# Kernel tuning notes

Measured on AMD Instinct MI355X. Metric: run time of the kernel, lower is better.

Reference implementation:

```python
import jax, jax.numpy as jnp
import numpy as np

C = 256
NUM_HEADS = 8
GROUPS = 8
EPS = 1e-5


def setup_inputs() -> dict:
    key = jax.random.key(0)
    ks = jax.random.split(key, 7)
    B, H, W = 2, 64, 64
    x = jax.random.normal(ks[0], (B, C, H, W), dtype=jnp.float32)
    gn_weight = jnp.ones((C,), dtype=jnp.float32)
    gn_bias = jnp.zeros((C,), dtype=jnp.float32)
    # 1x1 convs == per-pixel linear layers
    w_qkv = jax.random.normal(ks[1], (3 * C, C), dtype=jnp.float32) * (1.0 / np.sqrt(C))
    b_qkv = jax.random.normal(ks[2], (3 * C,), dtype=jnp.float32) * 0.01
    w_proj = jax.random.normal(ks[3], (C, C), dtype=jnp.float32) * (1.0 / np.sqrt(C))
    b_proj = jax.random.normal(ks[4], (C,), dtype=jnp.float32) * 0.01
    return {"x": x, "gn_weight": gn_weight, "gn_bias": gn_bias,
            "w_qkv": w_qkv, "b_qkv": b_qkv, "w_proj": w_proj, "b_proj": b_proj}


def reference(x, gn_weight, gn_bias, w_qkv, b_qkv, w_proj, b_proj):
    B, Cc, H, W = x.shape
    nh = NUM_HEADS
    hd = Cc // nh
    N = H * W
    scale = hd ** (-0.5)

    # GroupNorm(8, C): normalize over (C/G, H, W) per group, biased variance
    xg = x.reshape(B, GROUPS, Cc // GROUPS, H, W)
    mean = xg.mean(axis=(2, 3, 4), keepdims=True)
    var = xg.var(axis=(2, 3, 4), keepdims=True)
    hn = (xg - mean) * jax.lax.rsqrt(var + EPS)
    hn = hn.reshape(B, Cc, H, W) * gn_weight[None, :, None, None] + gn_bias[None, :, None, None]

    hf = hn.reshape(B, Cc, N)                       # [B, C, N]
    qkv = jnp.einsum('oc,bcn->bon', w_qkv, hf) + b_qkv[None, :, None]  # [B, 3C, N]
    qkv = qkv.reshape(B, 3, nh, hd, N)
    # q,k,v: [B, nh, N, hd]
    q = jnp.transpose(qkv[:, 0], (0, 1, 3, 2))
    k = jnp.transpose(qkv[:, 1], (0, 1, 3, 2))
    v = jnp.transpose(qkv[:, 2], (0, 1, 3, 2))

    attn = jnp.einsum('bhqd,bhkd->bhqk', q, k) * scale  # [B, nh, N, N]
    attn = jax.nn.softmax(attn, axis=-1)
    o = jnp.einsum('bhqk,bhkd->bhqd', attn, v)           # [B, nh, N, hd]
    o = jnp.transpose(o, (0, 1, 3, 2)).reshape(B, Cc, H, W)

    of = o.reshape(B, Cc, N)
    out = jnp.einsum('oc,bcn->bon', w_proj, of) + b_proj[None, :, None]
    return out.reshape(B, Cc, H, W)
```

## Files before the change

### kernel.cpp

```cpp
#include <hip/hip_runtime.h>


typedef _Float16 half8 __attribute__((ext_vector_type(8)));
typedef __fp16   fp16x2 __attribute__((ext_vector_type(2)));
typedef float    f32x4 __attribute__((ext_vector_type(4)));
typedef int      int2v __attribute__((ext_vector_type(2)));
typedef int      int4v __attribute__((ext_vector_type(4)));

__device__ __forceinline__ f32x4 mfma16(half8 a, half8 b, f32x4 c) {
  return __builtin_amdgcn_mfma_f32_16x16x32_f16(a, b, c, 0, 0, 0);
}

#if __has_builtin(__builtin_amdgcn_exp2f)
#define EXP2(x) __builtin_amdgcn_exp2f(x)
#else
#define EXP2(x) exp2f(x)
#endif

__device__ __forceinline__ unsigned short h_bits(_Float16 h) {
  return __builtin_bit_cast(unsigned short, h);
}
__device__ __forceinline__ int h2_bits(fp16x2 h) {
  return __builtin_bit_cast(int, h);
}

constexpr float CSCALE = (float)(1.4426950408889634 / 5.656854249492381);

__global__ __launch_bounds__(256) void gn_stats(const float* __restrict__ x,
                                                float* __restrict__ stats) {
  const int bg = blockIdx.x, ch = blockIdx.y, tid = threadIdx.x;
  const float* p = x + (size_t)bg * 131072 + (size_t)ch * 4096;
  float s = 0.f, ss = 0.f;
#pragma unroll
  for (int j = 0; j < 4; ++j) {
    f32x4 v = *(const f32x4*)(p + j * 1024 + tid * 4);
#pragma unroll
    for (int k = 0; k < 4; ++k) { s += v[k]; ss += v[k] * v[k]; }
  }
#pragma unroll
  for (int m = 1; m <= 32; m <<= 1) { s += __shfl_xor(s, m); ss += __shfl_xor(ss, m); }
  __shared__ float red[8];
  const int wv = tid >> 6;
  if ((tid & 63) == 0) { red[wv * 2] = s; red[wv * 2 + 1] = ss; }
  __syncthreads();
  if (tid == 0) {
    float S = red[0] + red[2] + red[4] + red[6];
    float SS = red[1] + red[3] + red[5] + red[7];
    atomicAdd(&stats[bg * 2], S);
    atomicAdd(&stats[bg * 2 + 1], SS);
  }
}

__global__ __launch_bounds__(256) void gn_apply(const float* __restrict__ x,
                                                const float* __restrict__ gw,
                                                const float* __restrict__ gb,
                                                const float* __restrict__ stats,
                                                _Float16* __restrict__ hn) {
  __shared__ float tile[64 * 65];
  const int tid = threadIdx.x;
  const int a = tid & 15;
  const int row16 = tid >> 4;
  const int b = blockIdx.z, c0 = blockIdx.y * 64, n0 = blockIdx.x * 64;
#pragma unroll
  for (int m = 0; m < 4; ++m) {
    const int cl = row16 + 16 * m;
    const int c = c0 + cl;
    const int g = c >> 5;
    const float s = stats[(b * 8 + g) * 2];
    const float ss = stats[(b * 8 + g) * 2 + 1];
    const float mean = s * (1.f / 131072.f);
    const float var = ss * (1.f / 131072.f) - mean * mean;
    const float rstd = rsqrtf(var + 1e-5f);
    const float ga = gw[c] * rstd;
    const float be = gb[c] - mean * ga;
    f32x4 xv = *(const f32x4*)(x + ((size_t)(b * 256 + c)) * 4096 + n0 + a * 4);
#pragma unroll
    for (int j = 0; j < 4; ++j) tile[cl * 65 + a * 4 + j] = xv[j] * ga + be;
  }
  __syncthreads();
#pragma unroll
  for (int m = 0; m < 4; ++m) {
    const int nl = row16 + 16 * m;
    const int cb = a * 4;
    int2v uh;
    unsigned short hh[4];
#pragma unroll
    for (int j = 0; j < 4; ++j) {
      hh[j] = h_bits((_Float16)tile[(cb + j) * 65 + nl]);
    }
    uh[0] = hh[0] | (hh[1] << 16); uh[1] = hh[2] | (hh[3] << 16);
    size_t off = ((size_t)(b * 4096 + n0 + nl)) * 256 + c0 + cb;
    *(int2v*)(hn + off) = uh;
  }
}

__global__ __launch_bounds__(256) void wcast(const float* __restrict__ wq,
                                             const float* __restrict__ wp,
                                             _Float16* __restrict__ wqh,
                                             _Float16* __restrict__ wph) {
  const int idx = blockIdx.x * 256 + threadIdx.x;
  if (idx < 196608) {
    wqh[idx] = (_Float16)wq[idx];
  } else {
    wph[idx - 196608] = (_Float16)wp[idx - 196608];
  }
}

template <int MODE>
__global__ __launch_bounds__(256) void gemm_f16(
    const _Float16* __restrict__ W, const _Float16* __restrict__ Bm,
    const float* __restrict__ bias,
    _Float16* __restrict__ qkT, _Float16* __restrict__ v_t,
    float* __restrict__ outp) {
  __shared__ _Float16 a_lds[2][4096];
  __shared__ _Float16 b_lds[2][4096];
  const int tid = threadIdx.x, lane = tid & 63, wv = tid >> 6;
  const int qq = lane >> 4, ii = lane & 15;
  const int m0 = blockIdx.x * 64, n0 = blockIdx.y * 64, bz = blockIdx.z;

  const _Float16* asrc[2];
  const _Float16* bsrc[2];
  int dst8[2];
#pragma unroll
  for (int rep = 0; rep < 2; ++rep) {
    const int idx = tid + 256 * rep;
    dst8[rep] = idx * 8;
    const int j = idx >> 7, c = (idx >> 6) & 1, l = idx & 63;
    const int lq = l >> 4, li = l & 15;
    asrc[rep] = W + (size_t)(m0 + 16 * j + li) * 256 + 32 * c + 8 * lq;
    bsrc[rep] = Bm + ((size_t)(bz * 4096 + n0 + 16 * j + li)) * 256 + 32 * c + 8 * lq;
  }

  f32x4 acc[4] = {};

  half8 ar0 = *(const half8*)asrc[0];
  half8 ar1 = *(const half8*)asrc[1];
  half8 br0 = *(const half8*)bsrc[0];
  half8 br1 = *(const half8*)bsrc[1];
  *(half8*)(a_lds[0] + dst8[0]) = ar0;
  *(half8*)(a_lds[0] + dst8[1]) = ar1;
  *(half8*)(b_lds[0] + dst8[0]) = br0;
  *(half8*)(b_lds[0] + dst8[1]) = br1;
  __syncthreads();

  for (int it = 0; it < 4; ++it) {
    const int cur = it & 1;
    if (it < 3) {
      const int ko = (it + 1) * 64;
      ar0 = *(const half8*)(asrc[0] + ko);
      ar1 = *(const half8*)(asrc[1] + ko);
      br0 = *(const half8*)(bsrc[0] + ko);
      br1 = *(const half8*)(bsrc[1] + ko);
    }
    half8 ah0 = *(const half8*)(a_lds[cur] + ((wv * 2 + 0) * 64 + lane) * 8);
    half8 ah1 = *(const half8*)(a_lds[cur] + ((wv * 2 + 1) * 64 + lane) * 8);
#pragma unroll
    for (int t = 0; t < 4; ++t) {
      half8 b0 = *(const half8*)(b_lds[cur] + ((t * 2 + 0) * 64 + lane) * 8);
      half8 b1 = *(const half8*)(b_lds[cur] + ((t * 2 + 1) * 64 + lane) * 8);
      acc[t] = mfma16(ah0, b0, acc[t]);
      acc[t] = mfma16(ah1, b1, acc[t]);
    }
    if (it < 3) {
      _Float16* an = a_lds[cur ^ 1];
      _Float16* bn = b_lds[cur ^ 1];
      *(half8*)(an + dst8[0]) = ar0;
      *(half8*)(an + dst8[1]) = ar1;
      *(half8*)(bn + dst8[0]) = br0;
      *(half8*)(bn + dst8[1]) = br1;
    }
    __syncthreads();
  }

  const int och0 = m0 + 16 * wv + 4 * qq;
  if (MODE == 0) {
    if (m0 < 512) {
      const float sc = (m0 < 256) ? CSCALE : 1.0f;
#pragma unroll
      for (int t = 0; t < 4; ++t) {
        const int n = n0 + 16 * t + ii;
        unsigned short hh[4];
#pragma unroll
        for (int r = 0; r < 4; ++r) {
          hh[r] = h_bits((_Float16)((acc[t][r] + bias[och0 + r]) * sc));
        }
        int2v u;
        u[0] = hh[0] | (hh[1] << 16);
        u[1] = hh[2] | (hh[3] << 16);
        *(int2v*)(qkT + ((size_t)(bz * 4096 + n)) * 512 + och0) = u;
      }
    } else {
#pragma unroll
      for (int t = 0; t < 4; ++t) {
#pragma unroll
        for (int r = 0; r < 4; ++r) {
          const int och = och0 + r;
          const int d = och - 512;
          const int hd_ = d & 31, head = d >> 5;
          const int n = n0 + 16 * t + ii;
          v_t[((size_t)((bz * 8 + head) * 32 + hd_)) * 4096 + n] =
              (_Float16)(acc[t][r] + bias[och]);
        }
      }
    }
  } else {
#pragma unroll
    for (int t = 0; t < 4; ++t) {
#pragma unroll
      for (int r = 0; r < 4; ++r) {
        const int och = och0 + r;
        const int n = n0 + 16 * t + ii;
        outp[((size_t)(bz * 256 + och)) * 4096 + n] = acc[t][r] + bias[och];
      }
    }
  }
}

__global__ __launch_bounds__(256) void attn_kernel(
    const _Float16* __restrict__ qkT, const _Float16* __restrict__ v_t,
    float* __restrict__ opart, float* __restrict__ lpart) {
  __shared__ _Float16 k_lds[2][4096];
  __shared__ _Float16 v_lds[2][4096];
  const int tid = threadIdx.x, lane = tid & 63, wv = tid >> 6;
  const int qq = lane >> 4, ii = lane & 15;
  const int bh = blockIdx.y, b = bh >> 3, h = bh & 7;
  const int n0 = blockIdx.x * 128;
  const int part = blockIdx.z;
  const int key0 = part * 2048;

  const _Float16* qbase =
      qkT + ((size_t)(b * 4096 + n0 + 32 * wv + ii)) * 512 + h * 32 + 8 * qq;
  half8 qf0 = *(const half8*)qbase;
  half8 qf1 = *(const half8*)(qbase + (size_t)16 * 512);

  const _Float16* ksrc[2];
  const _Float16* vsrc[2];
  int dst8[2];
#pragma unroll
  for (int rep = 0; rep < 2; ++rep) {
    const int idx = tid + 256 * rep;
    dst8[rep] = idx * 8;
    const int f = idx >> 6, l = idx & 63;
    const int fq = l >> 4, fi = l & 15;
    const int u = f >> 1, hf = f & 1;
    const int g = 32 * u + 4 * hf + 8 * (fi >> 2) + (fi & 3);
    ksrc[rep] = qkT + ((size_t)(b * 4096 + key0 + g)) * 512 + 256 + h * 32 + 8 * fq;
    vsrc[rep] = v_t + ((size_t)(bh * 32 + 16 * hf + fi)) * 4096 + key0 + 32 * u + 8 * fq;
  }

  half8 ones8;
#pragma unroll
  for (int j = 0; j < 8; ++j) ones8[j] = (_Float16)1.0f;

  f32x4 o00 = {}, o10 = {}, o01 = {}, o11 = {}, accl0 = {}, accl1 = {};

  half8 kr0 = *(const half8*)ksrc[0];
  half8 kr1 = *(const half8*)ksrc[1];
  half8 vr0 = *(const half8*)vsrc[0];
  half8 vr1 = *(const half8*)vsrc[1];
  *(half8*)(k_lds[0] + dst8[0]) = kr0;
  *(half8*)(k_lds[0] + dst8[1]) = kr1;
  *(half8*)(v_lds[0] + dst8[0]) = vr0;
  *(half8*)(v_lds[0] + dst8[1]) = vr1;
  __syncthreads();

  for (int kb = 0; kb < 16; ++kb) {
    const int cur = kb & 1;
    if (kb < 15) {
      const size_t ko = (size_t)(kb + 1) * 128 * 512;
      const size_t vo = (size_t)(kb + 1) * 128;
      kr0 = *(const half8*)(ksrc[0] + ko);
      kr1 = *(const half8*)(ksrc[1] + ko);
      vr0 = *(const half8*)(vsrc[0] + vo);
      vr1 = *(const half8*)(vsrc[1] + vo);
    }
    const _Float16* kbase = k_lds[cur];
    const _Float16* vbase = v_lds[cur];

#pragma unroll
    for (int u = 0; u < 4; ++u) {
      half8 kfa = *(const half8*)(kbase + u * 1024 + lane * 8);
      half8 kfb = *(const half8*)(kbase + u * 1024 + 512 + lane * 8);
      f32x4 z = {};
      f32x4 sa0 = mfma16(kfa, qf0, z);
      f32x4 sb0 = mfma16(kfb, qf0, z);
      f32x4 sa1 = mfma16(kfa, qf1, z);
      f32x4 sb1 = mfma16(kfb, qf1, z);
      int4v p0, p1;
      p0[0] = h2_bits(__builtin_amdgcn_cvt_pkrtz(EXP2(sa0[0]), EXP2(sa0[1])));
      p0[1] = h2_bits(__builtin_amdgcn_cvt_pkrtz(EXP2(sa0[2]), EXP2(sa0[3])));
      p0[2] = h2_bits(__builtin_amdgcn_cvt_pkrtz(EXP2(sb0[0]), EXP2(sb0[1])));
      p0[3] = h2_bits(__builtin_amdgcn_cvt_pkrtz(EXP2(sb0[2]), EXP2(sb0[3])));
      p1[0] = h2_bits(__builtin_amdgcn_cvt_pkrtz(EXP2(sa1[0]), EXP2(sa1[1])));
      p1[1] = h2_bits(__builtin_amdgcn_cvt_pkrtz(EXP2(sa1[2]), EXP2(sa1[3])));
      p1[2] = h2_bits(__builtin_amdgcn_cvt_pkrtz(EXP2(sb1[0]), EXP2(sb1[1])));
      p1[3] = h2_bits(__builtin_amdgcn_cvt_pkrtz(EXP2(sb1[2]), EXP2(sb1[3])));
      half8 pt0 = __builtin_bit_cast(half8, p0);
      half8 pt1 = __builtin_bit_cast(half8, p1);
      half8 vf0 = *(const half8*)(vbase + u * 1024 + lane * 8);
      half8 vf1 = *(const half8*)(vbase + u * 1024 + 512 + lane * 8);
      o00 = mfma16(vf0, pt0, o00);
      o10 = mfma16(vf1, pt0, o10);
      accl0 = mfma16(ones8, pt0, accl0);
      o01 = mfma16(vf0, pt1, o01);
      o11 = mfma16(vf1, pt1, o11);
      accl1 = mfma16(ones8, pt1, accl1);
    }

    if (kb < 15) {
      _Float16* kn = k_lds[cur ^ 1];
      _Float16* vn = v_lds[cur ^ 1];
      *(half8*)(kn + dst8[0]) = kr0;
      *(half8*)(kn + dst8[1]) = kr1;
      *(half8*)(vn + dst8[0]) = vr0;
      *(half8*)(vn + dst8[1]) = vr1;
    }
    __syncthreads();
  }

#pragma unroll
  for (int hf = 0; hf < 2; ++hf) {
    const f32x4 oa = hf ? o01 : o00;
    const f32x4 ob = hf ? o11 : o10;
    const int q = n0 + 32 * wv + 16 * hf + ii;
    float* base = opart + ((size_t)((part * 2 + b) * 4096 + q)) * 256 + h * 32;
    *(f32x4*)(base + 4 * qq) = oa;
    *(f32x4*)(base + 16 + 4 * qq) = ob;
    if (qq == 0) {
      lpart[((size_t)((part * 2 + b) * 4096 + q)) * 8 + h] = hf ? accl1[0] : accl0[0];
    }
  }
}

__global__ __launch_bounds__(256) void attn_combine(
    const float* __restrict__ opart, const float* __restrict__ lpart,
    _Float16* __restrict__ o16) {
  const int c = threadIdx.x, hh = c >> 5;
#pragma unroll
  for (int k = 0; k < 4; ++k) {
    const int row = blockIdx.x * 4 + k;
    const int b = row >> 12;
    const size_t i0 = ((size_t)(0 * 2 + b) * 4096 + (row & 4095)) * 256 + c;
    const size_t i1 = ((size_t)(1 * 2 + b) * 4096 + (row & 4095)) * 256 + c;
    const size_t l0i = ((size_t)(0 * 2 + b) * 4096 + (row & 4095)) * 8 + hh;
    const size_t l1i = ((size_t)(1 * 2 + b) * 4096 + (row & 4095)) * 8 + hh;
    const float O = opart[i0] + opart[i1];
    const float inv = 1.0f / (lpart[l0i] + lpart[l1i]);
    o16[(size_t)row * 256 + c] = (_Float16)(O * inv);
  }
}

extern "C" void kernel_launch(void* const* d_in, const int* in_sizes, int n_in,
                              void* d_out, int out_size, void* d_ws, size_t ws_size,
                              hipStream_t stream) {
  const float* x     = (const float*)d_in[0];
  const float* gnw   = (const float*)d_in[1];
  const float* gnb   = (const float*)d_in[2];
  const float* wqkv  = (const float*)d_in[3];
  const float* bqkv  = (const float*)d_in[4];
  const float* wproj = (const float*)d_in[5];
  const float* bproj = (const float*)d_in[6];
  float* out = (float*)d_out;

  char* ws = (char*)d_ws;
  size_t off = 0;
  auto alloc = [&](size_t bytes) -> char* {
    char* p = ws + off;
    off += (bytes + 255) & ~(size_t)255;
    return p;
  };
  float*    stats  = (float*)alloc(128);
  _Float16* hn     = (_Float16*)alloc((size_t)2 * 4096 * 256 * 2);
  _Float16* wq_h   = (_Float16*)alloc((size_t)768 * 256 * 2);
  _Float16* wp_h   = (_Float16*)alloc((size_t)256 * 256 * 2);
  _Float16* qkT    = (_Float16*)alloc((size_t)2 * 4096 * 512 * 2);
  _Float16* v_t    = (_Float16*)alloc((size_t)16 * 32 * 4096 * 2);
  float*    opart  = (float*)alloc((size_t)4 * 4096 * 256 * 4);
  float*    lpart  = (float*)alloc((size_t)4 * 4096 * 8 * 4);
  _Float16* o16 = hn;
  if (off > ws_size) return;

  (void)hipMemsetAsync(stats, 0, 256, stream);
  gn_stats<<<dim3(16, 32), 256, 0, stream>>>(x, stats);
  gn_apply<<<dim3(64, 4, 2), 256, 0, stream>>>(x, gnw, gnb, stats, hn);
  wcast<<<1024, 256, 0, stream>>>(wqkv, wproj, wq_h, wp_h);
  gemm_f16<0><<<dim3(12, 64, 2), 256, 0, stream>>>(wq_h, hn, bqkv, qkT, v_t,
                                                   nullptr);
  attn_kernel<<<dim3(32, 16, 2), 256, 0, stream>>>(qkT, v_t, opart, lpart);
  attn_combine<<<2048, 256, 0, stream>>>(opart, lpart, o16);
  gemm_f16<1><<<dim3(4, 64, 2), 256, 0, stream>>>(wp_h, o16, bproj, nullptr,
                                                  nullptr, out);
}
```

Measured before the change: 162.8 us.

## Split attention keys four ways, store fp16 partials, fuse weight cast into GEMM

```diff
diff --git a/kernel.cpp b/kernel.cpp
--- a/kernel.cpp
+++ b/kernel.cpp
@@ -23,8 +23,18 @@
 __device__ __forceinline__ int h2_bits(fp16x2 h) {
   return __builtin_bit_cast(int, h);
 }
+__device__ __forceinline__ half8 pack8(f32x4 lo, f32x4 hi) {
+  int4v u;
+  u[0] = h2_bits(__builtin_amdgcn_cvt_pkrtz(lo[0], lo[1]));
+  u[1] = h2_bits(__builtin_amdgcn_cvt_pkrtz(lo[2], lo[3]));
+  u[2] = h2_bits(__builtin_amdgcn_cvt_pkrtz(hi[0], hi[1]));
+  u[3] = h2_bits(__builtin_amdgcn_cvt_pkrtz(hi[2], hi[3]));
+  return __builtin_bit_cast(half8, u);
+}
 
 constexpr float CSCALE = (float)(1.4426950408889634 / 5.656854249492381);
+constexpr float VSCALE = 0.0009765625f;
+constexpr float VUNSC  = 1024.0f;
 
 __global__ __launch_bounds__(256) void gn_stats(const float* __restrict__ x,
                                                 float* __restrict__ stats) {
@@ -94,21 +104,9 @@
   }
 }
 
-__global__ __launch_bounds__(256) void wcast(const float* __restrict__ wq,
-                                             const float* __restrict__ wp,
-                                             _Float16* __restrict__ wqh,
-                                             _Float16* __restrict__ wph) {
-  const int idx = blockIdx.x * 256 + threadIdx.x;
-  if (idx < 196608) {
-    wqh[idx] = (_Float16)wq[idx];
-  } else {
-    wph[idx - 196608] = (_Float16)wp[idx - 196608];
-  }
-}
-
 template <int MODE>
 __global__ __launch_bounds__(256) void gemm_f16(
-    const _Float16* __restrict__ W, const _Float16* __restrict__ Bm,
+    const float* __restrict__ W, const _Float16* __restrict__ Bm,
     const float* __restrict__ bias,
     _Float16* __restrict__ qkT, _Float16* __restrict__ v_t,
     float* __restrict__ outp) {
@@ -118,7 +116,7 @@
   const int qq = lane >> 4, ii = lane & 15;
   const int m0 = blockIdx.x * 64, n0 = blockIdx.y * 64, bz = blockIdx.z;
 
-  const _Float16* asrc[2];
+  const float*    asrc[2];
   const _Float16* bsrc[2];
   int dst8[2];
 #pragma unroll
@@ -133,12 +131,12 @@
 
   f32x4 acc[4] = {};
 
-  half8 ar0 = *(const half8*)asrc[0];
-  half8 ar1 = *(const half8*)asrc[1];
+  f32x4 a0a = *(const f32x4*)asrc[0], a0b = *(const f32x4*)(asrc[0] + 4);
+  f32x4 a1a = *(const f32x4*)asrc[1], a1b = *(const f32x4*)(asrc[1] + 4);
   half8 br0 = *(const half8*)bsrc[0];
   half8 br1 = *(const half8*)bsrc[1];
-  *(half8*)(a_lds[0] + dst8[0]) = ar0;
-  *(half8*)(a_lds[0] + dst8[1]) = ar1;
+  *(half8*)(a_lds[0] + dst8[0]) = pack8(a0a, a0b);
+  *(half8*)(a_lds[0] + dst8[1]) = pack8(a1a, a1b);
   *(half8*)(b_lds[0] + dst8[0]) = br0;
   *(half8*)(b_lds[0] + dst8[1]) = br1;
   __syncthreads();
@@ -147,8 +145,10 @@
     const int cur = it & 1;
     if (it < 3) {
       const int ko = (it + 1) * 64;
-      ar0 = *(const half8*)(asrc[0] + ko);
-      ar1 = *(const half8*)(asrc[1] + ko);
+      a0a = *(const f32x4*)(asrc[0] + ko);
+      a0b = *(const f32x4*)(asrc[0] + ko + 4);
+      a1a = *(const f32x4*)(asrc[1] + ko);
+      a1b = *(const f32x4*)(asrc[1] + ko + 4);
       br0 = *(const half8*)(bsrc[0] + ko);
       br1 = *(const half8*)(bsrc[1] + ko);
     }
@@ -164,8 +164,8 @@
     if (it < 3) {
       _Float16* an = a_lds[cur ^ 1];
       _Float16* bn = b_lds[cur ^ 1];
-      *(half8*)(an + dst8[0]) = ar0;
-      *(half8*)(an + dst8[1]) = ar1;
+      *(half8*)(an + dst8[0]) = pack8(a0a, a0b);
+      *(half8*)(an + dst8[1]) = pack8(a1a, a1b);
       *(half8*)(bn + dst8[0]) = br0;
       *(half8*)(bn + dst8[1]) = br1;
     }
@@ -199,7 +199,7 @@
           const int hd_ = d & 31, head = d >> 5;
           const int n = n0 + 16 * t + ii;
           v_t[((size_t)((bz * 8 + head) * 32 + hd_)) * 4096 + n] =
-              (_Float16)(acc[t][r] + bias[och]);
+              (_Float16)((acc[t][r] + bias[och]) * VSCALE);
         }
       }
     }
@@ -216,37 +216,32 @@
   }
 }
 
-__global__ __launch_bounds__(256) void attn_kernel(
+__global__ __launch_bounds__(256, 8) void attn_kernel(
     const _Float16* __restrict__ qkT, const _Float16* __restrict__ v_t,
-    float* __restrict__ opart, float* __restrict__ lpart) {
-  __shared__ _Float16 k_lds[2][4096];
-  __shared__ _Float16 v_lds[2][4096];
+    _Float16* __restrict__ opart, float* __restrict__ lpart) {
+  __shared__ _Float16 k_lds[2][2048];
+  __shared__ _Float16 v_lds[2][2048];
   const int tid = threadIdx.x, lane = tid & 63, wv = tid >> 6;
   const int qq = lane >> 4, ii = lane & 15;
   const int bh = blockIdx.y, b = bh >> 3, h = bh & 7;
   const int n0 = blockIdx.x * 128;
   const int part = blockIdx.z;
-  const int key0 = part * 2048;
+  const int key0 = part * 1024;
 
   const _Float16* qbase =
       qkT + ((size_t)(b * 4096 + n0 + 32 * wv + ii)) * 512 + h * 32 + 8 * qq;
   half8 qf0 = *(const half8*)qbase;
   half8 qf1 = *(const half8*)(qbase + (size_t)16 * 512);
 
-  const _Float16* ksrc[2];
-  const _Float16* vsrc[2];
-  int dst8[2];
-#pragma unroll
-  for (int rep = 0; rep < 2; ++rep) {
-    const int idx = tid + 256 * rep;
-    dst8[rep] = idx * 8;
-    const int f = idx >> 6, l = idx & 63;
-    const int fq = l >> 4, fi = l & 15;
-    const int u = f >> 1, hf = f & 1;
-    const int g = 32 * u + 4 * hf + 8 * (fi >> 2) + (fi & 3);
-    ksrc[rep] = qkT + ((size_t)(b * 4096 + key0 + g)) * 512 + 256 + h * 32 + 8 * fq;
-    vsrc[rep] = v_t + ((size_t)(bh * 32 + 16 * hf + fi)) * 4096 + key0 + 32 * u + 8 * fq;
-  }
+  const int f = tid >> 6, l = tid & 63;
+  const int fq = l >> 4, fi = l & 15;
+  const int u0 = f >> 1, hf = f & 1;
+  const int g = 32 * u0 + 4 * hf + 8 * (fi >> 2) + (fi & 3);
+  const _Float16* ksrc =
+      qkT + ((size_t)(b * 4096 + key0 + g)) * 512 + 256 + h * 32 + 8 * fq;
+  const _Float16* vsrc =
+      v_t + ((size_t)(bh * 32 + 16 * hf + fi)) * 4096 + key0 + 32 * u0 + 8 * fq;
+  const int dst8 = tid * 8;
 
   half8 ones8;
 #pragma unroll
@@ -254,31 +249,23 @@
 
   f32x4 o00 = {}, o10 = {}, o01 = {}, o11 = {}, accl0 = {}, accl1 = {};
 
-  half8 kr0 = *(const half8*)ksrc[0];
-  half8 kr1 = *(const half8*)ksrc[1];
-  half8 vr0 = *(const half8*)vsrc[0];
-  half8 vr1 = *(const half8*)vsrc[1];
-  *(half8*)(k_lds[0] + dst8[0]) = kr0;
-  *(half8*)(k_lds[0] + dst8[1]) = kr1;
-  *(half8*)(v_lds[0] + dst8[0]) = vr0;
-  *(half8*)(v_lds[0] + dst8[1]) = vr1;
+  half8 kr = *(const half8*)ksrc;
+  half8 vr = *(const half8*)vsrc;
+  *(half8*)(k_lds[0] + dst8) = kr;
+  *(half8*)(v_lds[0] + dst8) = vr;
   __syncthreads();
 
   for (int kb = 0; kb < 16; ++kb) {
     const int cur = kb & 1;
     if (kb < 15) {
-      const size_t ko = (size_t)(kb + 1) * 128 * 512;
-      const size_t vo = (size_t)(kb + 1) * 128;
-      kr0 = *(const half8*)(ksrc[0] + ko);
-      kr1 = *(const half8*)(ksrc[1] + ko);
-      vr0 = *(const half8*)(vsrc[0] + vo);
-      vr1 = *(const half8*)(vsrc[1] + vo);
+      kr = *(const half8*)(ksrc + (size_t)(kb + 1) * 64 * 512);
+      vr = *(const half8*)(vsrc + (size_t)(kb + 1) * 64);
     }
     const _Float16* kbase = k_lds[cur];
     const _Float16* vbase = v_lds[cur];
 
 #pragma unroll
-    for (int u = 0; u < 4; ++u) {
+    for (int u = 0; u < 2; ++u) {
       half8 kfa = *(const half8*)(kbase + u * 1024 + lane * 8);
       half8 kfb = *(const half8*)(kbase + u * 1024 + 512 + lane * 8);
       f32x4 z = {};
@@ -308,45 +295,51 @@
     }
 
     if (kb < 15) {
-      _Float16* kn = k_lds[cur ^ 1];
-      _Float16* vn = v_lds[cur ^ 1];
-      *(half8*)(kn + dst8[0]) = kr0;
-      *(half8*)(kn + dst8[1]) = kr1;
-      *(half8*)(vn + dst8[0]) = vr0;
-      *(half8*)(vn + dst8[1]) = vr1;
+      *(half8*)(k_lds[cur ^ 1] + dst8) = kr;
+      *(half8*)(v_lds[cur ^ 1] + dst8) = vr;
     }
     __syncthreads();
   }
 
 #pragma unroll
-  for (int hf = 0; hf < 2; ++hf) {
-    const f32x4 oa = hf ? o01 : o00;
-    const f32x4 ob = hf ? o11 : o10;
-    const int q = n0 + 32 * wv + 16 * hf + ii;
-    float* base = opart + ((size_t)((part * 2 + b) * 4096 + q)) * 256 + h * 32;
-    *(f32x4*)(base + 4 * qq) = oa;
-    *(f32x4*)(base + 16 + 4 * qq) = ob;
+  for (int hfq = 0; hfq < 2; ++hfq) {
+    const f32x4 oa = hfq ? o01 : o00;
+    const f32x4 ob = hfq ? o11 : o10;
+    const int q = n0 + 32 * wv + 16 * hfq + ii;
+    _Float16* base =
+        opart + ((size_t)((part * 2 + b) * 4096 + q)) * 256 + h * 32;
+    unsigned short hh[4];
+#pragma unroll
+    for (int r = 0; r < 4; ++r) hh[r] = h_bits((_Float16)oa[r]);
+    int2v ua;
+    ua[0] = hh[0] | (hh[1] << 16); ua[1] = hh[2] | (hh[3] << 16);
+    *(int2v*)(base + 4 * qq) = ua;
+#pragma unroll
+    for (int r = 0; r < 4; ++r) hh[r] = h_bits((_Float16)ob[r]);
+    ua[0] = hh[0] | (hh[1] << 16); ua[1] = hh[2] | (hh[3] << 16);
+    *(int2v*)(base + 16 + 4 * qq) = ua;
     if (qq == 0) {
-      lpart[((size_t)((part * 2 + b) * 4096 + q)) * 8 + h] = hf ? accl1[0] : accl0[0];
+      lpart[((size_t)((part * 2 + b) * 4096 + q)) * 8 + h] =
+          hfq ? accl1[0] : accl0[0];
     }
   }
 }
 
 __global__ __launch_bounds__(256) void attn_combine(
-    const float* __restrict__ opart, const float* __restrict__ lpart,
+    const _Float16* __restrict__ opart, const float* __restrict__ lpart,
     _Float16* __restrict__ o16) {
   const int c = threadIdx.x, hh = c >> 5;
 #pragma unroll
   for (int k = 0; k < 4; ++k) {
     const int row = blockIdx.x * 4 + k;
-    const int b = row >> 12;
-    const size_t i0 = ((size_t)(0 * 2 + b) * 4096 + (row & 4095)) * 256 + c;
-    const size_t i1 = ((size_t)(1 * 2 + b) * 4096 + (row & 4095)) * 256 + c;
-    const size_t l0i = ((size_t)(0 * 2 + b) * 4096 + (row & 4095)) * 8 + hh;
-    const size_t l1i = ((size_t)(1 * 2 + b) * 4096 + (row & 4095)) * 8 + hh;
-    const float O = opart[i0] + opart[i1];
-    const float inv = 1.0f / (lpart[l0i] + lpart[l1i]);
-    o16[(size_t)row * 256 + c] = (_Float16)(O * inv);
+    const int b = row >> 12, q = row & 4095;
+    float O = 0.f, L = 0.f;
+#pragma unroll
+    for (int p = 0; p < 4; ++p) {
+      O += (float)opart[((size_t)((p * 2 + b) * 4096 + q)) * 256 + c];
+      L += lpart[((size_t)((p * 2 + b) * 4096 + q)) * 8 + hh];
+    }
+    o16[(size_t)row * 256 + c] = (_Float16)(O * (VUNSC / L));
   }
 }
 
@@ -371,23 +364,20 @@
   };
   float*    stats  = (float*)alloc(128);
   _Float16* hn     = (_Float16*)alloc((size_t)2 * 4096 * 256 * 2);
-  _Float16* wq_h   = (_Float16*)alloc((size_t)768 * 256 * 2);
-  _Float16* wp_h   = (_Float16*)alloc((size_t)256 * 256 * 2);
   _Float16* qkT    = (_Float16*)alloc((size_t)2 * 4096 * 512 * 2);
   _Float16* v_t    = (_Float16*)alloc((size_t)16 * 32 * 4096 * 2);
-  float*    opart  = (float*)alloc((size_t)4 * 4096 * 256 * 4);
-  float*    lpart  = (float*)alloc((size_t)4 * 4096 * 8 * 4);
+  _Float16* opart  = (_Float16*)alloc((size_t)8 * 4096 * 256 * 2);
+  float*    lpart  = (float*)alloc((size_t)8 * 4096 * 8 * 4);
   _Float16* o16 = hn;
   if (off > ws_size) return;
 
   (void)hipMemsetAsync(stats, 0, 256, stream);
   gn_stats<<<dim3(16, 32), 256, 0, stream>>>(x, stats);
   gn_apply<<<dim3(64, 4, 2), 256, 0, stream>>>(x, gnw, gnb, stats, hn);
-  wcast<<<1024, 256, 0, stream>>>(wqkv, wproj, wq_h, wp_h);
-  gemm_f16<0><<<dim3(12, 64, 2), 256, 0, stream>>>(wq_h, hn, bqkv, qkT, v_t,
+  gemm_f16<0><<<dim3(12, 64, 2), 256, 0, stream>>>(wqkv, hn, bqkv, qkT, v_t,
                                                    nullptr);
-  attn_kernel<<<dim3(32, 16, 2), 256, 0, stream>>>(qkT, v_t, opart, lpart);
+  attn_kernel<<<dim3(32, 16, 4), 256, 0, stream>>>(qkT, v_t, opart, lpart);
   attn_combine<<<2048, 256, 0, stream>>>(opart, lpart, o16);
-  gemm_f16<1><<<dim3(4, 64, 2), 256, 0, stream>>>(wp_h, o16, bproj, nullptr,
+  gemm_f16<1><<<dim3(4, 64, 2), 256, 0, stream>>>(wproj, o16, bproj, nullptr,
                                                   nullptr, out);
 }
```

Result: slower. 166.1 us (+2.0%).
